# Kernel optimization log

Hardware: AMD Instinct MI355X
Metric: run time of the kernel (lower is better)

The kernel has to match this reference:

```python
import math
import jax, jax.numpy as jnp
import numpy as np

B, TQ, TK, D = 32, 1024, 1024, 64


def setup_inputs() -> dict:
    key = jax.random.key(0)
    ks = jax.random.split(key, 6)
    return {
        "queries": jax.random.normal(ks[0], (B, TQ, D), dtype=jnp.float32),
        "keys": jax.random.normal(ks[1], (B, TK, D), dtype=jnp.float32),
        "values": jax.random.normal(ks[2], (B, TK, D), dtype=jnp.float32),
        "pos_k": jax.random.normal(ks[3], (TQ, TK, D), dtype=jnp.float32),
        "pos_v": jax.random.normal(ks[4], (TQ, TK, D), dtype=jnp.float32),
        "valid_lens": jax.random.randint(ks[5], (B,), 1, TK + 1, dtype=jnp.int32),
    }


def reference(queries, keys, values, pos_k, pos_v, valid_lens):
    d = queries.shape[-1]
    # content scores: [B, Tq, Tk]
    scores = jnp.einsum("bqd,bkd->bqk", queries, keys)
    # relative-position key scores: per query position q, Q[:,q,:] @ pos_k[q].T
    scores_pos = jnp.einsum("bqd,qkd->bqk", queries, pos_k)
    scores = (scores + scores_pos) / math.sqrt(d)
    # masked softmax: positions >= valid_len set to -1e6 (as in the torch code)
    key_idx = jnp.arange(scores.shape[-1])  # [Tk]
    mask = key_idx[None, None, :] < valid_lens[:, None, None]  # [B,1,Tk]
    scores = jnp.where(mask, scores, jnp.float32(-1e6))
    attn = jax.nn.softmax(scores, axis=-1)  # [B, Tq, Tk]
    # value aggregation + relative-position value aggregation
    output = jnp.einsum("bqk,bkd->bqd", attn, values)
    output_pos = jnp.einsum("bqk,qkd->bqd", attn, pos_v)
    return output + output_pos
```

## Files before the change

### kernel.cpp

```cpp
#include <hip/hip_runtime.h>

typedef _Float16 f16;
typedef _Float16 f16x2 __attribute__((ext_vector_type(2)));
typedef _Float16 f16x4 __attribute__((ext_vector_type(4)));
typedef _Float16 f16x8 __attribute__((ext_vector_type(8)));
typedef float f32x4 __attribute__((ext_vector_type(4)));

constexpr int TQn = 1024, TKn = 1024, Dn = 64, Bn = 32;
constexpr int NB = 8;
constexpr int NQ = 16;
constexpr int KT = 32;
constexpr int NSTEP = TKn / KT;

constexpr int KROW  = 136;
constexpr int KTILE = KT * KROW;
constexpr int LK    = 0;
constexpr int LPK   = NB * KTILE;
constexpr int VTROW = 72;
constexpr int VTILE = Dn * VTROW;
constexpr int LVT   = 0;
constexpr int LPVT  = NB * VTILE;
constexpr int OPS   = LPVT + NQ * VTILE;
constexpr int LS    = OPS;
constexpr int SROWF = 34;
constexpr int LMo   = LS + 128 * 136;
constexpr int LLo   = LMo + 512;
constexpr int LAo   = LLo + 512;
constexpr int LVLq  = LAo + 512;
constexpr int SMEMB = LVLq + 32;
constexpr int OROWF = 68;

union F4 { float4 v; float a[4]; };

__device__ __forceinline__ f16x8 ld8(const void* p) {
  f16x4 a = *(const f16x4*)p;
  f16x4 b = *(const f16x4*)((const char*)p + 8);
  return __builtin_shufflevector(a, b, 0, 1, 2, 3, 4, 5, 6, 7);
}
__device__ __forceinline__ f16x4 cvt4(float4 x) {
  f16x4 r; r[0] = (f16)x.x; r[1] = (f16)x.y; r[2] = (f16)x.z; r[3] = (f16)x.w;
  return r;
}

__global__ __launch_bounds__(512, 2)
void attn_rpr_mfma(const float* __restrict__ Qg, const float* __restrict__ Kg,
                   const float* __restrict__ Vg, const float* __restrict__ PKg,
                   const float* __restrict__ PVg, const int* __restrict__ VLg,
                   float* __restrict__ Og) {
  __shared__ __align__(16) char sm[SMEMB];
  float* const sM  = (float*)(sm + LMo);
  float* const sL  = (float*)(sm + LLo);
  float* const sA  = (float*)(sm + LAo);
  int*   const sVL = (int*)(sm + LVLq);
  float* const sS  = (float*)(sm + LS);

  const int tid = (int)threadIdx.x;
  const int w = tid >> 6, l = tid & 63;
  const int l16 = l & 15, g = l >> 4;
  const int qt = (int)blockIdx.x, bg = (int)blockIdx.y;
  const int q0 = qt * NQ, b0 = bg * NB;

  if (tid < 128) { sM[tid] = -3.0e38f; sL[tid] = 0.0f; }
  if (tid < NB) sVL[tid] = VLg[b0 + tid];

  f16x8 aQc[2], aQp[2][2];
  {
    const float* qr = Qg + ((size_t)(b0 + w) * TQn + (q0 + l16)) * Dn;
#pragma unroll
    for (int c = 0; c < 2; ++c) {
      float4 x = *(const float4*)(qr + c * 32 + g * 8);
      float4 y = *(const float4*)(qr + c * 32 + g * 8 + 4);
      aQc[c] = __builtin_shufflevector(cvt4(x), cvt4(y), 0, 1, 2, 3, 4, 5, 6, 7);
    }
    const int bp = l16 & 7;
    const bool vld = (l16 < 8);
#pragma unroll
    for (int qi = 0; qi < 2; ++qi) {
      const float* qp = Qg + ((size_t)(b0 + bp) * TQn + (q0 + 2 * w + qi)) * Dn;
#pragma unroll
      for (int c = 0; c < 2; ++c) {
        float4 x = *(const float4*)(qp + c * 32 + g * 8);
        float4 y = *(const float4*)(qp + c * 32 + g * 8 + 4);
        if (!vld) { x = make_float4(0.f, 0.f, 0.f, 0.f); y = make_float4(0.f, 0.f, 0.f, 0.f); }
        aQp[qi][c] = __builtin_shufflevector(cvt4(x), cvt4(y), 0, 1, 2, 3, 4, 5, 6, 7);
      }
    }
  }
  __syncthreads();

  int vmax = 0;
#pragma unroll
  for (int i = 0; i < NB; ++i) vmax = max(vmax, sVL[i]);

  const f32x4 z4 = {0.f, 0.f, 0.f, 0.f};
  f32x4 Oc[4], Op[2][4];
#pragma unroll
  for (int n = 0; n < 4; ++n) { Oc[n] = z4; Op[0][n] = z4; Op[1][n] = z4; }

#pragma unroll 1
  for (int t = 0; t < NSTEP; ++t) {
    const int k0 = t * KT;
    if (k0 >= vmax) break;

#pragma unroll
    for (int i = 0; i < 4; ++i) {
      const int gg = tid + 512 * i;
      const int d8 = gg & 7, kk = (gg >> 3) & 31, b = gg >> 8;
      const float* src = Kg + ((size_t)(b0 + b) * TKn + (k0 + kk)) * Dn + d8 * 8;
      float4 x = *(const float4*)src, y = *(const float4*)(src + 4);
      char* dst = sm + LK + b * KTILE + kk * KROW + d8 * 16;
      *(f16x4*)dst = cvt4(x);
      *(f16x4*)(dst + 8) = cvt4(y);
    }
#pragma unroll
    for (int i = 0; i < 8; ++i) {
      const int gg = tid + 512 * i;
      const int d8 = gg & 7, kk = (gg >> 3) & 31, q = gg >> 8;
      const float* src = PKg + ((size_t)(q0 + q) * TKn + (k0 + kk)) * Dn + d8 * 8;
      float4 x = *(const float4*)src, y = *(const float4*)(src + 4);
      char* dst = sm + LPK + q * KTILE + kk * KROW + d8 * 16;
      *(f16x4*)dst = cvt4(x);
      *(f16x4*)(dst + 8) = cvt4(y);
    }
    __syncthreads();

    f32x4 Cc[2], Cp[2][2];
#pragma unroll
    for (int n = 0; n < 2; ++n) { Cc[n] = z4; Cp[0][n] = z4; Cp[1][n] = z4; }
#pragma unroll
    for (int c = 0; c < 2; ++c)
#pragma unroll
      for (int n = 0; n < 2; ++n) {
        f16x8 bf = ld8(sm + LK + w * KTILE + (n * 16 + l16) * KROW + c * 64 + g * 16);
        Cc[n] = __builtin_amdgcn_mfma_f32_16x16x32_f16(aQc[c], bf, Cc[n], 0, 0, 0);
      }
#pragma unroll
    for (int qi = 0; qi < 2; ++qi)
#pragma unroll
      for (int c = 0; c < 2; ++c)
#pragma unroll
        for (int n = 0; n < 2; ++n) {
          f16x8 bf = ld8(sm + LPK + (2 * w + qi) * KTILE + (n * 16 + l16) * KROW + c * 64 + g * 16);
          Cp[qi][n] = __builtin_amdgcn_mfma_f32_16x16x32_f16(aQp[qi][c], bf, Cp[qi][n], 0, 0, 0);
        }
#pragma unroll
    for (int n = 0; n < 2; ++n)
#pragma unroll
      for (int r = 0; r < 4; ++r)
        sS[(w * 16 + g * 4 + r) * SROWF + n * 16 + l16] = Cc[n][r];
    __syncthreads();
#pragma unroll
    for (int qi = 0; qi < 2; ++qi)
#pragma unroll
      for (int n = 0; n < 2; ++n)
#pragma unroll
        for (int r = 0; r < 4; ++r) {
          const int rowb = g * 4 + r;
          if (rowb < 8)
            sS[(rowb * 16 + 2 * w + qi) * SROWF + n * 16 + l16] += Cp[qi][n][r];
        }
    __syncthreads();

    {
      const int r = tid >> 2, j4 = tid & 3;
      const float* srow = sS + r * SROWF + j4 * 8;
      const int vl = sVL[r >> 4];
      float v[8];
#pragma unroll
      for (int jj = 0; jj < 8; ++jj) {
        const float s = srow[jj] * 0.125f;
        v[jj] = (k0 + j4 * 8 + jj < vl) ? s : -1.0e6f;
      }
      float mloc = v[0];
#pragma unroll
      for (int jj = 1; jj < 8; ++jj) mloc = fmaxf(mloc, v[jj]);
      mloc = fmaxf(mloc, __shfl_xor(mloc, 1));
      mloc = fmaxf(mloc, __shfl_xor(mloc, 2));
      const float mo = sM[r];
      const float mn = fmaxf(mo, mloc);
      float pv[8], ps = 0.f;
#pragma unroll
      for (int jj = 0; jj < 8; ++jj) { pv[jj] = __expf(v[jj] - mn); ps += pv[jj]; }
      ps += __shfl_xor(ps, 1);
      ps += __shfl_xor(ps, 2);
      if (j4 == 0) {
        const float al = __expf(mo - mn);
        sM[r] = mn; sA[r] = al;
        sL[r] = sL[r] * al + ps;
      }
      f16x4 p0, p1;
#pragma unroll
      for (int jj = 0; jj < 4; ++jj) { p0[jj] = (f16)pv[jj]; p1[jj] = (f16)pv[4 + jj]; }
      *(f16x4*)(sm + LS + r * 136 + j4 * 16) = p0;
      *(f16x4*)(sm + LS + r * 136 + j4 * 16 + 8) = p1;
    }

#pragma unroll
    for (int i = 0; i < 4; ++i) {
      const int p = tid + 512 * i;
      const int d4 = p & 15, kk2 = (p >> 4) & 15, b = p >> 8;
      const float* src = Vg + ((size_t)(b0 + b) * TKn + (k0 + 2 * kk2)) * Dn + d4 * 4;
      F4 r0, r1; r0.v = *(const float4*)src; r1.v = *(const float4*)(src + Dn);
      char* base = sm + LVT + b * VTILE + kk2 * 4;
#pragma unroll
      for (int j = 0; j < 4; ++j) {
        f16x2 t2; t2[0] = (f16)r0.a[j]; t2[1] = (f16)r1.a[j];
        *(f16x2*)(base + (d4 * 4 + j) * VTROW) = t2;
      }
    }
#pragma unroll
    for (int i = 0; i < 8; ++i) {
      const int p = tid + 512 * i;
      const int d4 = p & 15, kk2 = (p >> 4) & 15, q = p >> 8;
      const float* src = PVg + ((size_t)(q0 + q) * TKn + (k0 + 2 * kk2)) * Dn + d4 * 4;
      F4 r0, r1; r0.v = *(const float4*)src; r1.v = *(const float4*)(src + Dn);
      char* base = sm + LPVT + q * VTILE + kk2 * 4;
#pragma unroll
      for (int j = 0; j < 4; ++j) {
        f16x2 t2; t2[0] = (f16)r0.a[j]; t2[1] = (f16)r1.a[j];
        *(f16x2*)(base + (d4 * 4 + j) * VTROW) = t2;
      }
    }
    __syncthreads();

    {
      float alC[4], alP0[4], alP1[4];
#pragma unroll
      for (int r = 0; r < 4; ++r) {
        alC[r] = sA[w * 16 + g * 4 + r];
        const int rb = (g * 4 + r) & 7;
        alP0[r] = sA[rb * 16 + 2 * w];
        alP1[r] = sA[rb * 16 + 2 * w + 1];
      }
#pragma unroll
      for (int n = 0; n < 4; ++n)
#pragma unroll
        for (int r = 0; r < 4; ++r) {
          Oc[n][r] *= alC[r];
          Op[0][n][r] *= alP0[r];
          Op[1][n][r] *= alP1[r];
        }
      const f16x8 aPc = ld8(sm + LS + (w * 16 + l16) * 136 + g * 16);
      f16x8 aPp[2];
#pragma unroll
      for (int qi = 0; qi < 2; ++qi) {
        if (l16 < 8) aPp[qi] = ld8(sm + LS + (l16 * 16 + 2 * w + qi) * 136 + g * 16);
        else { f16x8 z = {0, 0, 0, 0, 0, 0, 0, 0}; aPp[qi] = z; }
      }
#pragma unroll
      for (int n = 0; n < 4; ++n) {
        f16x8 bf = ld8(sm + LVT + w * VTILE + (n * 16 + l16) * VTROW + g * 16);
        Oc[n] = __builtin_amdgcn_mfma_f32_16x16x32_f16(aPc, bf, Oc[n], 0, 0, 0);
      }
#pragma unroll
      for (int qi = 0; qi < 2; ++qi)
#pragma unroll
        for (int n = 0; n < 4; ++n) {
          f16x8 bf = ld8(sm + LPVT + (2 * w + qi) * VTILE + (n * 16 + l16) * VTROW + g * 16);
          Op[qi][n] = __builtin_amdgcn_mfma_f32_16x16x32_f16(aPp[qi], bf, Op[qi][n], 0, 0, 0);
        }
    }
    __syncthreads();
  }

  float* const sO = (float*)(sm + LVT);
#pragma unroll
  for (int qi = 0; qi < 2; ++qi)
#pragma unroll
    for (int n = 0; n < 4; ++n)
#pragma unroll
      for (int r = 0; r < 4; ++r) {
        const int rowb = g * 4 + r;
        if (rowb < 8)
          sO[(rowb * 16 + 2 * w + qi) * OROWF + n * 16 + l16] = Op[qi][n][r];
      }
  __syncthreads();
#pragma unroll
  for (int n = 0; n < 4; ++n)
#pragma unroll
    for (int r = 0; r < 4; ++r) {
      const int q = g * 4 + r;
      const int rr = w * 16 + q;
      const float val = (Oc[n][r] + sO[rr * OROWF + n * 16 + l16]) / sL[rr];
      Og[((size_t)(b0 + w) * TQn + (q0 + q)) * Dn + n * 16 + l16] = val;
    }
}

extern "C" void kernel_launch(void* const* d_in, const int* in_sizes, int n_in,
                              void* d_out, int out_size, void* d_ws, size_t ws_size,
                              hipStream_t stream) {
  (void)in_sizes; (void)n_in; (void)out_size; (void)d_ws; (void)ws_size;
  const float* Qg  = (const float*)d_in[0];
  const float* Kg  = (const float*)d_in[1];
  const float* Vg  = (const float*)d_in[2];
  const float* PKg = (const float*)d_in[3];
  const float* PVg = (const float*)d_in[4];
  const int*   VLg = (const int*)d_in[5];
  float* Og = (float*)d_out;

  dim3 grid(TQn / NQ, Bn / NB, 1);
  dim3 block(512, 1, 1);
  hipLaunchKernelGGL(attn_rpr_mfma, grid, block, 0, stream, Qg, Kg, Vg, PKg, PVg, VLg, Og);
}
```

Measured before the change: 884.5 us.

## Split keys four ways with larger batch/query tiles and a combine kernel

Each block now covers 16 batches by 32 queries, doubling reuse of every pos_k/pos_v tile across batches. The key range is split four ways along grid.z, with a new combine kernel merging the partial outputs via per-row max and sum. The key tile shrinks to 16, and P@V now uses 16x16x16 MFMAs. Softmax state is kept in registers, one row per thread. The extra partial-output workspace traffic and second launch add cost, and the larger per-block register and LDS footprint may limit occupancy.

```diff
diff --git a/kernel.cpp b/kernel.cpp
--- a/kernel.cpp
+++ b/kernel.cpp
@@ -7,28 +7,26 @@
 typedef float f32x4 __attribute__((ext_vector_type(4)));
 
 constexpr int TQn = 1024, TKn = 1024, Dn = 64, Bn = 32;
-constexpr int NB = 8;
-constexpr int NQ = 16;
-constexpr int KT = 32;
-constexpr int NSTEP = TKn / KT;
+constexpr int NB = 16;
+constexpr int NQ = 32;
+constexpr int KT = 16;
+constexpr int NSPLIT = 4;
+constexpr int KRANGE = TKn / NSPLIT;
+constexpr int NSTEP = KRANGE / KT;
 
 constexpr int KROW  = 136;
 constexpr int KTILE = KT * KROW;
 constexpr int LK    = 0;
 constexpr int LPK   = NB * KTILE;
-constexpr int VTROW = 72;
+constexpr int VTROW = 36;
 constexpr int VTILE = Dn * VTROW;
 constexpr int LVT   = 0;
 constexpr int LPVT  = NB * VTILE;
-constexpr int OPS   = LPVT + NQ * VTILE;
-constexpr int LS    = OPS;
-constexpr int SROWF = 34;
-constexpr int LMo   = LS + 128 * 136;
-constexpr int LLo   = LMo + 512;
-constexpr int LAo   = LLo + 512;
-constexpr int LVLq  = LAo + 512;
-constexpr int SMEMB = LVLq + 32;
-constexpr int OROWF = 68;
+constexpr int OPSEND = 110592;
+constexpr int LS    = OPSEND;
+constexpr int SSTR  = 72;
+constexpr int LAo   = LS + 512 * SSTR;
+constexpr int SMEMB = LAo + 2048;
 
 union F4 { float4 v; float a[4]; };
 
@@ -37,259 +35,283 @@
   f16x4 b = *(const f16x4*)((const char*)p + 8);
   return __builtin_shufflevector(a, b, 0, 1, 2, 3, 4, 5, 6, 7);
 }
+__device__ __forceinline__ f16x4 ld4u(const void* p) {
+  union { uint u[2]; f16x4 h; } x;
+  x.u[0] = *(const uint*)p; x.u[1] = *(const uint*)((const char*)p + 4);
+  return x.h;
+}
 __device__ __forceinline__ f16x4 cvt4(float4 x) {
   f16x4 r; r[0] = (f16)x.x; r[1] = (f16)x.y; r[2] = (f16)x.z; r[3] = (f16)x.w;
   return r;
 }
 
 __global__ __launch_bounds__(512, 2)
-void attn_rpr_mfma(const float* __restrict__ Qg, const float* __restrict__ Kg,
-                   const float* __restrict__ Vg, const float* __restrict__ PKg,
-                   const float* __restrict__ PVg, const int* __restrict__ VLg,
-                   float* __restrict__ Og) {
+void attn_fwd(const float* __restrict__ Qg, const float* __restrict__ Kg,
+              const float* __restrict__ Vg, const float* __restrict__ PKg,
+              const float* __restrict__ PVg, const int* __restrict__ VLg,
+              float* __restrict__ Ows, float* __restrict__ Mws, float* __restrict__ Lws) {
   __shared__ __align__(16) char sm[SMEMB];
-  float* const sM  = (float*)(sm + LMo);
-  float* const sL  = (float*)(sm + LLo);
-  float* const sA  = (float*)(sm + LAo);
-  int*   const sVL = (int*)(sm + LVLq);
-  float* const sS  = (float*)(sm + LS);
+  float* const sS = (float*)(sm + LS);
+  float* const sA = (float*)(sm + LAo);
 
   const int tid = (int)threadIdx.x;
-  const int w = tid >> 6, l = tid & 63;
+  const int w = tid >> 6;
+  const int l = tid & 63;
   const int l16 = l & 15, g = l >> 4;
-  const int qt = (int)blockIdx.x, bg = (int)blockIdx.y;
+  const int qt = (int)blockIdx.x, bg = (int)blockIdx.y, ks = (int)blockIdx.z;
   const int q0 = qt * NQ, b0 = bg * NB;
-
-  if (tid < 128) { sM[tid] = -3.0e38f; sL[tid] = 0.0f; }
-  if (tid < NB) sVL[tid] = VLg[b0 + tid];
-
-  f16x8 aQc[2], aQp[2][2];
-  {
-    const float* qr = Qg + ((size_t)(b0 + w) * TQn + (q0 + l16)) * Dn;
+  const int kbase = ks * KRANGE;
+
+  f16x8 aC[2][2][2];
+  f16x8 aP[4][2];
+#pragma unroll
+  for (int i = 0; i < 2; ++i)
+#pragma unroll
+    for (int mt = 0; mt < 2; ++mt) {
+      const float* qr = Qg + ((size_t)(b0 + 2 * w + i) * TQn + (q0 + mt * 16 + l16)) * Dn;
+#pragma unroll
+      for (int c = 0; c < 2; ++c) {
+        float4 x = *(const float4*)(qr + c * 32 + g * 8);
+        float4 y = *(const float4*)(qr + c * 32 + g * 8 + 4);
+        aC[i][mt][c] = __builtin_shufflevector(cvt4(x), cvt4(y), 0, 1, 2, 3, 4, 5, 6, 7);
+      }
+    }
+#pragma unroll
+  for (int qq = 0; qq < 4; ++qq) {
+    const float* qr = Qg + ((size_t)(b0 + l16) * TQn + (q0 + 4 * w + qq)) * Dn;
 #pragma unroll
     for (int c = 0; c < 2; ++c) {
       float4 x = *(const float4*)(qr + c * 32 + g * 8);
       float4 y = *(const float4*)(qr + c * 32 + g * 8 + 4);
-      aQc[c] = __builtin_shufflevector(cvt4(x), cvt4(y), 0, 1, 2, 3, 4, 5, 6, 7);
-    }
-    const int bp = l16 & 7;
-    const bool vld = (l16 < 8);
-#pragma unroll
-    for (int qi = 0; qi < 2; ++qi) {
-      const float* qp = Qg + ((size_t)(b0 + bp) * TQn + (q0 + 2 * w + qi)) * Dn;
-#pragma unroll
-      for (int c = 0; c < 2; ++c) {
-        float4 x = *(const float4*)(qp + c * 32 + g * 8);
-        float4 y = *(const float4*)(qp + c * 32 + g * 8 + 4);
-        if (!vld) { x = make_float4(0.f, 0.f, 0.f, 0.f); y = make_float4(0.f, 0.f, 0.f, 0.f); }
-        aQp[qi][c] = __builtin_shufflevector(cvt4(x), cvt4(y), 0, 1, 2, 3, 4, 5, 6, 7);
-      }
-    }
-  }
+      aP[qq][c] = __builtin_shufflevector(cvt4(x), cvt4(y), 0, 1, 2, 3, 4, 5, 6, 7);
+    }
+  }
+
+  int vmax = 0;
+#pragma unroll
+  for (int i = 0; i < NB; ++i) vmax = max(vmax, VLg[b0 + i]);
+  const int vl_row = VLg[b0 + (tid >> 5)];
+
+  const int d4 = tid & 15, kc = (tid >> 4) & 15, bb = tid >> 8;
+  const float* Kt  = Kg  + ((size_t)(b0 + bb) * TKn + kc) * Dn + d4 * 4;
+  const float* PKt = PKg + ((size_t)(q0 + bb) * TKn + kc) * Dn + d4 * 4;
+  char* const dK  = sm + LK  + bb * KTILE + kc * KROW + d4 * 8;
+  char* const dPK = sm + LPK + bb * KTILE + kc * KROW + d4 * 8;
+  const int k2 = tid & 7, dv = (tid >> 3) & 15, bv = tid >> 7;
+  const float* Vt  = Vg  + ((size_t)(b0 + bv) * TKn + 2 * k2) * Dn + dv * 4;
+  const float* PVt = PVg + ((size_t)(q0 + bv) * TKn + 2 * k2) * Dn + dv * 4;
+  char* const dV  = sm + LVT  + bv * VTILE + k2 * 4;
+  char* const dPV = sm + LPVT + bv * VTILE + k2 * 4;
+
+  const f32x4 z4 = {0.f, 0.f, 0.f, 0.f};
+  f32x4 Oc[2][2][4], Op[4][4];
+#pragma unroll
+  for (int n = 0; n < 4; ++n) {
+#pragma unroll
+    for (int i = 0; i < 2; ++i) { Oc[i][0][n] = z4; Oc[i][1][n] = z4; }
+#pragma unroll
+    for (int qq = 0; qq < 4; ++qq) Op[qq][n] = z4;
+  }
+  float m_run = -3.0e38f, l_run = 0.0f;
+
   __syncthreads();
-
-  int vmax = 0;
-#pragma unroll
-  for (int i = 0; i < NB; ++i) vmax = max(vmax, sVL[i]);
-
-  const f32x4 z4 = {0.f, 0.f, 0.f, 0.f};
-  f32x4 Oc[4], Op[2][4];
-#pragma unroll
-  for (int n = 0; n < 4; ++n) { Oc[n] = z4; Op[0][n] = z4; Op[1][n] = z4; }
 
 #pragma unroll 1
   for (int t = 0; t < NSTEP; ++t) {
-    const int k0 = t * KT;
+    const int k0 = kbase + t * KT;
     if (k0 >= vmax) break;
-
+    const int kof = k0 * Dn;
+
+#pragma unroll
+    for (int i = 0; i < 8; ++i) {
+      float4 v = *(const float4*)(Kt + kof + i * 131072);
+      *(f16x4*)(dK + i * (2 * KTILE)) = cvt4(v);
+    }
+#pragma unroll
+    for (int i = 0; i < 16; ++i) {
+      float4 v = *(const float4*)(PKt + kof + i * 131072);
+      *(f16x4*)(dPK + i * (2 * KTILE)) = cvt4(v);
+    }
+    __syncthreads();
+
+    f32x4 Cp[4];
+#pragma unroll
+    for (int qq = 0; qq < 4; ++qq) Cp[qq] = z4;
+#pragma unroll
+    for (int i = 0; i < 2; ++i) {
+      const f16x8 bf0 = ld8(sm + LK + (2 * w + i) * KTILE + l16 * KROW + g * 16);
+      const f16x8 bf1 = ld8(sm + LK + (2 * w + i) * KTILE + l16 * KROW + 64 + g * 16);
+#pragma unroll
+      for (int mt = 0; mt < 2; ++mt) {
+        f32x4 acc = z4;
+        acc = __builtin_amdgcn_mfma_f32_16x16x32_f16(aC[i][mt][0], bf0, acc, 0, 0, 0);
+        acc = __builtin_amdgcn_mfma_f32_16x16x32_f16(aC[i][mt][1], bf1, acc, 0, 0, 0);
+#pragma unroll
+        for (int rr = 0; rr < 4; ++rr)
+          sS[((2 * w + i) * 32 + mt * 16 + g * 4 + rr) * (SSTR / 4) + l16] = acc[rr];
+      }
+    }
+#pragma unroll
+    for (int qq = 0; qq < 4; ++qq) {
+      const f16x8 bf0 = ld8(sm + LPK + (4 * w + qq) * KTILE + l16 * KROW + g * 16);
+      const f16x8 bf1 = ld8(sm + LPK + (4 * w + qq) * KTILE + l16 * KROW + 64 + g * 16);
+      Cp[qq] = __builtin_amdgcn_mfma_f32_16x16x32_f16(aP[qq][0], bf0, Cp[qq], 0, 0, 0);
+      Cp[qq] = __builtin_amdgcn_mfma_f32_16x16x32_f16(aP[qq][1], bf1, Cp[qq], 0, 0, 0);
+    }
+    __syncthreads();
+
+#pragma unroll
+    for (int qq = 0; qq < 4; ++qq)
+#pragma unroll
+      for (int rr = 0; rr < 4; ++rr)
+        sS[((g * 4 + rr) * 32 + 4 * w + qq) * (SSTR / 4) + l16] += Cp[qq][rr];
 #pragma unroll
     for (int i = 0; i < 4; ++i) {
-      const int gg = tid + 512 * i;
-      const int d8 = gg & 7, kk = (gg >> 3) & 31, b = gg >> 8;
-      const float* src = Kg + ((size_t)(b0 + b) * TKn + (k0 + kk)) * Dn + d8 * 8;
-      float4 x = *(const float4*)src, y = *(const float4*)(src + 4);
-      char* dst = sm + LK + b * KTILE + kk * KROW + d8 * 16;
-      *(f16x4*)dst = cvt4(x);
-      *(f16x4*)(dst + 8) = cvt4(y);
-    }
-#pragma unroll
-    for (int i = 0; i < 8; ++i) {
-      const int gg = tid + 512 * i;
-      const int d8 = gg & 7, kk = (gg >> 3) & 31, q = gg >> 8;
-      const float* src = PKg + ((size_t)(q0 + q) * TKn + (k0 + kk)) * Dn + d8 * 8;
-      float4 x = *(const float4*)src, y = *(const float4*)(src + 4);
-      char* dst = sm + LPK + q * KTILE + kk * KROW + d8 * 16;
-      *(f16x4*)dst = cvt4(x);
-      *(f16x4*)(dst + 8) = cvt4(y);
-    }
-    __syncthreads();
-
-    f32x4 Cc[2], Cp[2][2];
-#pragma unroll
-    for (int n = 0; n < 2; ++n) { Cc[n] = z4; Cp[0][n] = z4; Cp[1][n] = z4; }
-#pragma unroll
-    for (int c = 0; c < 2; ++c)
-#pragma unroll
-      for (int n = 0; n < 2; ++n) {
-        f16x8 bf = ld8(sm + LK + w * KTILE + (n * 16 + l16) * KROW + c * 64 + g * 16);
-        Cc[n] = __builtin_amdgcn_mfma_f32_16x16x32_f16(aQc[c], bf, Cc[n], 0, 0, 0);
-      }
-#pragma unroll
-    for (int qi = 0; qi < 2; ++qi)
-#pragma unroll
-      for (int c = 0; c < 2; ++c)
-#pragma unroll
-        for (int n = 0; n < 2; ++n) {
-          f16x8 bf = ld8(sm + LPK + (2 * w + qi) * KTILE + (n * 16 + l16) * KROW + c * 64 + g * 16);
-          Cp[qi][n] = __builtin_amdgcn_mfma_f32_16x16x32_f16(aQp[qi][c], bf, Cp[qi][n], 0, 0, 0);
-        }
-#pragma unroll
-    for (int n = 0; n < 2; ++n)
-#pragma unroll
-      for (int r = 0; r < 4; ++r)
-        sS[(w * 16 + g * 4 + r) * SROWF + n * 16 + l16] = Cc[n][r];
-    __syncthreads();
-#pragma unroll
-    for (int qi = 0; qi < 2; ++qi)
-#pragma unroll
-      for (int n = 0; n < 2; ++n)
-#pragma unroll
-        for (int r = 0; r < 4; ++r) {
-          const int rowb = g * 4 + r;
-          if (rowb < 8)
-            sS[(rowb * 16 + 2 * w + qi) * SROWF + n * 16 + l16] += Cp[qi][n][r];
-        }
-    __syncthreads();
-
-    {
-      const int r = tid >> 2, j4 = tid & 3;
-      const float* srow = sS + r * SROWF + j4 * 8;
-      const int vl = sVL[r >> 4];
-      float v[8];
-#pragma unroll
-      for (int jj = 0; jj < 8; ++jj) {
-        const float s = srow[jj] * 0.125f;
-        v[jj] = (k0 + j4 * 8 + jj < vl) ? s : -1.0e6f;
-      }
-      float mloc = v[0];
-#pragma unroll
-      for (int jj = 1; jj < 8; ++jj) mloc = fmaxf(mloc, v[jj]);
-      mloc = fmaxf(mloc, __shfl_xor(mloc, 1));
-      mloc = fmaxf(mloc, __shfl_xor(mloc, 2));
-      const float mo = sM[r];
-      const float mn = fmaxf(mo, mloc);
-      float pv[8], ps = 0.f;
-#pragma unroll
-      for (int jj = 0; jj < 8; ++jj) { pv[jj] = __expf(v[jj] - mn); ps += pv[jj]; }
-      ps += __shfl_xor(ps, 1);
-      ps += __shfl_xor(ps, 2);
-      if (j4 == 0) {
-        const float al = __expf(mo - mn);
-        sM[r] = mn; sA[r] = al;
-        sL[r] = sL[r] * al + ps;
-      }
-      f16x4 p0, p1;
-#pragma unroll
-      for (int jj = 0; jj < 4; ++jj) { p0[jj] = (f16)pv[jj]; p1[jj] = (f16)pv[4 + jj]; }
-      *(f16x4*)(sm + LS + r * 136 + j4 * 16) = p0;
-      *(f16x4*)(sm + LS + r * 136 + j4 * 16 + 8) = p1;
-    }
-
-#pragma unroll
-    for (int i = 0; i < 4; ++i) {
-      const int p = tid + 512 * i;
-      const int d4 = p & 15, kk2 = (p >> 4) & 15, b = p >> 8;
-      const float* src = Vg + ((size_t)(b0 + b) * TKn + (k0 + 2 * kk2)) * Dn + d4 * 4;
-      F4 r0, r1; r0.v = *(const float4*)src; r1.v = *(const float4*)(src + Dn);
-      char* base = sm + LVT + b * VTILE + kk2 * 4;
+      F4 r0, r1;
+      r0.v = *(const float4*)(Vt + kof + i * 262144);
+      r1.v = *(const float4*)(Vt + kof + i * 262144 + Dn);
+      char* base = dV + i * (4 * VTILE);
 #pragma unroll
       for (int j = 0; j < 4; ++j) {
         f16x2 t2; t2[0] = (f16)r0.a[j]; t2[1] = (f16)r1.a[j];
-        *(f16x2*)(base + (d4 * 4 + j) * VTROW) = t2;
+        *(f16x2*)(base + (dv * 4 + j) * VTROW) = t2;
       }
     }
 #pragma unroll
     for (int i = 0; i < 8; ++i) {
-      const int p = tid + 512 * i;
-      const int d4 = p & 15, kk2 = (p >> 4) & 15, q = p >> 8;
-      const float* src = PVg + ((size_t)(q0 + q) * TKn + (k0 + 2 * kk2)) * Dn + d4 * 4;
-      F4 r0, r1; r0.v = *(const float4*)src; r1.v = *(const float4*)(src + Dn);
-      char* base = sm + LPVT + q * VTILE + kk2 * 4;
+      F4 r0, r1;
+      r0.v = *(const float4*)(PVt + kof + i * 262144);
+      r1.v = *(const float4*)(PVt + kof + i * 262144 + Dn);
+      char* base = dPV + i * (4 * VTILE);
 #pragma unroll
       for (int j = 0; j < 4; ++j) {
         f16x2 t2; t2[0] = (f16)r0.a[j]; t2[1] = (f16)r1.a[j];
-        *(f16x2*)(base + (d4 * 4 + j) * VTROW) = t2;
+        *(f16x2*)(base + (dv * 4 + j) * VTROW) = t2;
       }
     }
     __syncthreads();
 
     {
-      float alC[4], alP0[4], alP1[4];
-#pragma unroll
-      for (int r = 0; r < 4; ++r) {
-        alC[r] = sA[w * 16 + g * 4 + r];
-        const int rb = (g * 4 + r) & 7;
-        alP0[r] = sA[rb * 16 + 2 * w];
-        alP1[r] = sA[rb * 16 + 2 * w + 1];
-      }
-#pragma unroll
-      for (int n = 0; n < 4; ++n)
-#pragma unroll
-        for (int r = 0; r < 4; ++r) {
-          Oc[n][r] *= alC[r];
-          Op[0][n][r] *= alP0[r];
-          Op[1][n][r] *= alP1[r];
+      float* row = sS + tid * (SSTR / 4);
+      float v[16]; float mloc = -3.0e38f;
+#pragma unroll
+      for (int j = 0; j < 16; ++j) {
+        const float s = row[j] * 0.125f;
+        v[j] = (k0 + j < vl_row) ? s : -1.0e6f;
+        mloc = fmaxf(mloc, v[j]);
+      }
+      const float mn = fmaxf(m_run, mloc);
+      float ps = 0.f; f16 ph[16];
+#pragma unroll
+      for (int j = 0; j < 16; ++j) { const float p = __expf(v[j] - mn); ps += p; ph[j] = (f16)p; }
+      const float al = __expf(m_run - mn);
+      m_run = mn; l_run = l_run * al + ps;
+      sA[tid] = al;
+#pragma unroll
+      for (int j = 0; j < 4; ++j) {
+        f16x4 pk; pk[0] = ph[4 * j]; pk[1] = ph[4 * j + 1]; pk[2] = ph[4 * j + 2]; pk[3] = ph[4 * j + 3];
+        *(f16x4*)((char*)row + j * 8) = pk;
+      }
+    }
+    __syncthreads();
+
+    {
+#pragma unroll
+      for (int i = 0; i < 2; ++i)
+#pragma unroll
+        for (int mt = 0; mt < 2; ++mt)
+#pragma unroll
+          for (int rr = 0; rr < 4; ++rr) {
+            const float al = sA[(2 * w + i) * 32 + mt * 16 + g * 4 + rr];
+#pragma unroll
+            for (int n = 0; n < 4; ++n) Oc[i][mt][n][rr] *= al;
+          }
+#pragma unroll
+      for (int qq = 0; qq < 4; ++qq)
+#pragma unroll
+        for (int rr = 0; rr < 4; ++rr) {
+          const float al = sA[(g * 4 + rr) * 32 + 4 * w + qq];
+#pragma unroll
+          for (int n = 0; n < 4; ++n) Op[qq][n][rr] *= al;
         }
-      const f16x8 aPc = ld8(sm + LS + (w * 16 + l16) * 136 + g * 16);
-      f16x8 aPp[2];
-#pragma unroll
-      for (int qi = 0; qi < 2; ++qi) {
-        if (l16 < 8) aPp[qi] = ld8(sm + LS + (l16 * 16 + 2 * w + qi) * 136 + g * 16);
-        else { f16x8 z = {0, 0, 0, 0, 0, 0, 0, 0}; aPp[qi] = z; }
-      }
-#pragma unroll
-      for (int n = 0; n < 4; ++n) {
-        f16x8 bf = ld8(sm + LVT + w * VTILE + (n * 16 + l16) * VTROW + g * 16);
-        Oc[n] = __builtin_amdgcn_mfma_f32_16x16x32_f16(aPc, bf, Oc[n], 0, 0, 0);
-      }
-#pragma unroll
-      for (int qi = 0; qi < 2; ++qi)
+#pragma unroll
+      for (int i = 0; i < 2; ++i) {
+        f16x4 pa[2];
+#pragma unroll
+        for (int mt = 0; mt < 2; ++mt)
+          pa[mt] = *(const f16x4*)(sm + LS + ((2 * w + i) * 32 + mt * 16 + l16) * SSTR + g * 8);
 #pragma unroll
         for (int n = 0; n < 4; ++n) {
-          f16x8 bf = ld8(sm + LPVT + (2 * w + qi) * VTILE + (n * 16 + l16) * VTROW + g * 16);
-          Op[qi][n] = __builtin_amdgcn_mfma_f32_16x16x32_f16(aPp[qi], bf, Op[qi][n], 0, 0, 0);
+          const f16x4 bf = ld4u(sm + LVT + (2 * w + i) * VTILE + (n * 16 + l16) * VTROW + g * 8);
+#pragma unroll
+          for (int mt = 0; mt < 2; ++mt)
+            Oc[i][mt][n] = __builtin_amdgcn_mfma_f32_16x16x16f16(pa[mt], bf, Oc[i][mt][n], 0, 0, 0);
         }
-    }
-    __syncthreads();
-  }
-
-  float* const sO = (float*)(sm + LVT);
-#pragma unroll
-  for (int qi = 0; qi < 2; ++qi)
+      }
+#pragma unroll
+      for (int qq = 0; qq < 4; ++qq) {
+        const f16x4 pa = *(const f16x4*)(sm + LS + (l16 * 32 + 4 * w + qq) * SSTR + g * 8);
+#pragma unroll
+        for (int n = 0; n < 4; ++n) {
+          const f16x4 bf = ld4u(sm + LPVT + (4 * w + qq) * VTILE + (n * 16 + l16) * VTROW + g * 8);
+          Op[qq][n] = __builtin_amdgcn_mfma_f32_16x16x16f16(pa, bf, Op[qq][n], 0, 0, 0);
+        }
+      }
+    }
+    __syncthreads();
+  }
+
+  float* const sO = (float*)sm;
+#pragma unroll
+  for (int qq = 0; qq < 4; ++qq)
 #pragma unroll
     for (int n = 0; n < 4; ++n)
 #pragma unroll
-      for (int r = 0; r < 4; ++r) {
-        const int rowb = g * 4 + r;
-        if (rowb < 8)
-          sO[(rowb * 16 + 2 * w + qi) * OROWF + n * 16 + l16] = Op[qi][n][r];
-      }
+      for (int rr = 0; rr < 4; ++rr)
+        sO[((g * 4 + rr) * 32 + 4 * w + qq) * 68 + n * 16 + l16] = Op[qq][n][rr];
   __syncthreads();
 #pragma unroll
-  for (int n = 0; n < 4; ++n)
-#pragma unroll
-    for (int r = 0; r < 4; ++r) {
-      const int q = g * 4 + r;
-      const int rr = w * 16 + q;
-      const float val = (Oc[n][r] + sO[rr * OROWF + n * 16 + l16]) / sL[rr];
-      Og[((size_t)(b0 + w) * TQn + (q0 + q)) * Dn + n * 16 + l16] = val;
-    }
+  for (int i = 0; i < 2; ++i)
+#pragma unroll
+    for (int mt = 0; mt < 2; ++mt)
+#pragma unroll
+      for (int rr = 0; rr < 4; ++rr) {
+        const int rloc = (2 * w + i) * 32 + mt * 16 + g * 4 + rr;
+        float* dst = Ows + (((size_t)ks * Bn + (b0 + 2 * w + i)) * TQn + (q0 + mt * 16 + g * 4 + rr)) * Dn;
+#pragma unroll
+        for (int n = 0; n < 4; ++n)
+          dst[n * 16 + l16] = Oc[i][mt][n][rr] + sO[rloc * 68 + n * 16 + l16];
+      }
+  {
+    const size_t idx = ((size_t)ks * Bn + (b0 + (tid >> 5))) * TQn + (q0 + (tid & 31));
+    Mws[idx] = m_run; Lws[idx] = l_run;
+  }
+}
+
+__global__ __launch_bounds__(256)
+void combine4(const float* __restrict__ Ows, const float* __restrict__ Mws,
+              const float* __restrict__ Lws, float* __restrict__ Og) {
+  const int gid = (int)blockIdx.x * 256 + (int)threadIdx.x;
+  const int d = gid & 63;
+  const int row = gid >> 6;
+  float m[NSPLIT], lv[NSPLIT];
+#pragma unroll
+  for (int s = 0; s < NSPLIT; ++s) { m[s] = Mws[s * 32768 + row]; lv[s] = Lws[s * 32768 + row]; }
+  float M = fmaxf(fmaxf(m[0], m[1]), fmaxf(m[2], m[3]));
+  float L = 0.f, o = 0.f;
+#pragma unroll
+  for (int s = 0; s < NSPLIT; ++s) {
+    const float wgt = __expf(m[s] - M);
+    L += wgt * lv[s];
+    o += wgt * Ows[((size_t)s * 32768 + row) * 64 + d];
+  }
+  Og[(size_t)row * 64 + d] = o / L;
 }
 
 extern "C" void kernel_launch(void* const* d_in, const int* in_sizes, int n_in,
                               void* d_out, int out_size, void* d_ws, size_t ws_size,
                               hipStream_t stream) {
-  (void)in_sizes; (void)n_in; (void)out_size; (void)d_ws; (void)ws_size;
+  (void)in_sizes; (void)n_in; (void)out_size; (void)ws_size;
   const float* Qg  = (const float*)d_in[0];
   const float* Kg  = (const float*)d_in[1];
   const float* Vg  = (const float*)d_in[2];
@@ -298,7 +320,16 @@
   const int*   VLg = (const int*)d_in[5];
   float* Og = (float*)d_out;
 
-  dim3 grid(TQn / NQ, Bn / NB, 1);
+  float* ws  = (float*)d_ws;
+  float* Ows = ws;
+  float* Mws = ws + 8388608;
+  float* Lws = ws + 8519680;
+
+  dim3 grid(TQn / NQ, Bn / NB, NSPLIT);
   dim3 block(512, 1, 1);
-  hipLaunchKernelGGL(attn_rpr_mfma, grid, block, 0, stream, Qg, Kg, Vg, PKg, PVg, VLg, Og);
-}
+  hipLaunchKernelGGL(attn_fwd, grid, block, 0, stream, Qg, Kg, Vg, PKg, PVg, VLg, Ows, Mws, Lws);
+
+  dim3 cgrid((Bn * TQn * Dn) / 256, 1, 1);
+  dim3 cblock(256, 1, 1);
+  hipLaunchKernelGGL(combine4, cgrid, cblock, 0, stream, Ows, Mws, Lws, Og);
+}
```

After: 803.6 us. -9.2%, faster.
